# Optimization experiments

Hardware: AMD Instinct MI355X
Metric: run time of the kernel (lower is better)

## Reference

```python
import jax, jax.numpy as jnp
import numpy as np

# BiAttn: additive (concat-based) cross attention.
# Original torch: e = Linear([k_i ; q_j]) = k_i @ W[:H] + q_j @ W[H:] + b  (separable)
# a = softmax(e, axis=-1 over Y); out[b,x,h] = sum_y v[b,y,h] * a[b,x,y]

B, X, Y, H = 8, 2048, 2048, 1024


def setup_inputs() -> dict:
    key = jax.random.key(0)
    kq, kk, kv, kw = jax.random.split(key, 4)
    q = jax.random.normal(kq, (B, Y, H), dtype=jnp.float32)
    k = jax.random.normal(kk, (B, X, H), dtype=jnp.float32)
    v = jax.random.normal(kv, (B, Y, H), dtype=jnp.float32)
    W = jax.random.normal(kw, (2 * H,), dtype=jnp.float32) * (1.0 / np.sqrt(2 * H))
    b = jnp.zeros((), dtype=jnp.float32)
    return {"q": q, "k": k, "v": v, "W": W, "b": b}


def reference(q, k, v, W, b):
    Hdim = k.shape[-1]
    Wk, Wq = W[:Hdim], W[Hdim:]
    # Separable additive score: e[b,x,y] = k[b,x]@Wk + q[b,y]@Wq + b
    sk = jnp.einsum('bxh,h->bx', k, Wk)          # [B, X]
    sq = jnp.einsum('byh,h->by', q, Wq)          # [B, Y]
    e = sk[:, :, None] + sq[:, None, :] + b      # [B, X, Y]
    a = jax.nn.softmax(e, axis=-1)               # softmax over Y
    out = jnp.einsum('byh,bxy->bxh', v, a)       # [B, X, H]
    return out
```

## Files before the change

### kernel.cpp

```cpp
#include <hip/hip_runtime.h>

#define Bn 8
#define Xn 2048
#define Yn 2048
#define Hn 1024
#define YC 8
#define NCH (Yn / YC)

__global__ __launch_bounds__(256, 8)
void k_fused(const float* __restrict__ q, const float* __restrict__ W,
             const float* __restrict__ v,
             float* __restrict__ o_part, float* __restrict__ s_part) {
    const int b = blockIdx.y;
    const int c = blockIdx.x;
    const int y0 = c * YC;
    const int t = threadIdx.x;
    const int wave = t >> 6, lane = t & 63;
    __shared__ float pe[YC];

    const float4* w4 = (const float4*)(W + Hn);
    const float4 ww0 = w4[lane];
    const float4 ww1 = w4[lane + 64];
    const float4 ww2 = w4[lane + 128];
    const float4 ww3 = w4[lane + 192];

    {
        const int ra = wave * 2;
        const float4* qa = (const float4*)(q + ((size_t)b * Yn + y0 + ra) * Hn);
        const float4* qb = qa + (Hn / 4);
        float acca = 0.f, accb = 0.f;
        #pragma unroll
        for (int i = 0; i < 4; ++i) {
            float4 a  = qa[lane + 64 * i];
            float4 bb = qb[lane + 64 * i];
            float4 w  = (i == 0) ? ww0 : (i == 1) ? ww1 : (i == 2) ? ww2 : ww3;
            acca += a.x * w.x + a.y * w.y + a.z * w.z + a.w * w.w;
            accb += bb.x * w.x + bb.y * w.y + bb.z * w.z + bb.w * w.w;
        }
        #pragma unroll
        for (int off = 32; off > 0; off >>= 1) {
            acca += __shfl_xor(acca, off, 64);
            accb += __shfl_xor(accb, off, 64);
        }
        if (lane == 0) {
            pe[ra]     = __expf(acca);
            pe[ra + 1] = __expf(accb);
        }
    }
    __syncthreads();

    const float4* v4 = (const float4*)(v + ((size_t)b * Yn + y0) * Hn);
    float4 acc = {0.f, 0.f, 0.f, 0.f};
    #pragma unroll
    for (int yy = 0; yy < YC; ++yy) {
        const float pw = pe[yy];
        const float4 vv = v4[(size_t)yy * (Hn / 4) + t];
        acc.x = fmaf(pw, vv.x, acc.x);
        acc.y = fmaf(pw, vv.y, acc.y);
        acc.z = fmaf(pw, vv.z, acc.z);
        acc.w = fmaf(pw, vv.w, acc.w);
    }
    ((float4*)o_part)[((size_t)c * Bn + b) * (Hn / 4) + t] = acc;

    if (t == 0) {
        float s = 0.f;
        #pragma unroll
        for (int i = 0; i < YC; ++i) s += pe[i];
        s_part[c * Bn + b] = s;
    }
}

__global__ void k_red(const float* __restrict__ o_part,
                      const float* __restrict__ s_part,
                      float* __restrict__ o_final) {
    const int idx = blockIdx.x * 256 + threadIdx.x;
    const int b = idx >> 10;
    const int h = idx & (Hn - 1);
    float acc = 0.f, s = 0.f;
    #pragma unroll 8
    for (int c = 0; c < NCH; ++c) {
        acc += o_part[(size_t)(c * Bn + b) * Hn + h];
        s   += s_part[c * Bn + b];
    }
    o_final[idx] = acc / s;
}

__global__ void k_bcast(const float* __restrict__ o, float4* __restrict__ out) {
    const size_t i = (size_t)blockIdx.x * blockDim.x + threadIdx.x;
    const int h4 = (int)(i & (Hn / 4 - 1));
    const size_t row = i >> 8;
    const int b = (int)(row >> 11);
    const float4* o4 = (const float4*)o;
    out[i] = o4[b * (Hn / 4) + h4];
}

extern "C" void kernel_launch(void* const* d_in, const int* in_sizes, int n_in,
                              void* d_out, int out_size, void* d_ws, size_t ws_size,
                              hipStream_t stream) {
    const float* q = (const float*)d_in[0];
    const float* v = (const float*)d_in[2];
    const float* W = (const float*)d_in[3];
    float* out = (float*)d_out;

    float* o_part = (float*)d_ws;
    float* s_part = o_part + (size_t)NCH * Bn * Hn;
    float* o_fin  = s_part + NCH * Bn;

    k_fused<<<dim3(NCH, Bn), 256, 0, stream>>>(q, W, v, o_part, s_part);
    k_red  <<<Bn * Hn / 256, 256, 0, stream>>>(o_part, s_part, o_fin);
    k_bcast<<<(Bn * (size_t)Xn * Hn / 4) / 256, 256, 0, stream>>>(o_fin, (float4*)out);
}
```

Baseline: 216.9 us.

## Split score computation from PV accumulation and enlarge Y chunk per block

```diff
diff --git a/kernel.cpp b/kernel.cpp
--- a/kernel.cpp
+++ b/kernel.cpp
@@ -4,19 +4,18 @@
 #define Xn 2048
 #define Yn 2048
 #define Hn 1024
-#define YC 8
+#define RPB 8
+#define YC 32
 #define NCH (Yn / YC)
 
-__global__ __launch_bounds__(256, 8)
-void k_fused(const float* __restrict__ q, const float* __restrict__ W,
-             const float* __restrict__ v,
-             float* __restrict__ o_part, float* __restrict__ s_part) {
-    const int b = blockIdx.y;
-    const int c = blockIdx.x;
-    const int y0 = c * YC;
+
+__global__ __launch_bounds__(256)
+void k_pe(const float* __restrict__ q, const float* __restrict__ W,
+          float* __restrict__ pe, float* __restrict__ sb) {
+    const int blk = blockIdx.x;
     const int t = threadIdx.x;
     const int wave = t >> 6, lane = t & 63;
-    __shared__ float pe[YC];
+    __shared__ float ps[RPB];
 
     const float4* w4 = (const float4*)(W + Hn);
     const float4 ww0 = w4[lane];
@@ -24,65 +23,87 @@
     const float4 ww2 = w4[lane + 128];
     const float4 ww3 = w4[lane + 192];
 
-    {
-        const int ra = wave * 2;
-        const float4* qa = (const float4*)(q + ((size_t)b * Yn + y0 + ra) * Hn);
-        const float4* qb = qa + (Hn / 4);
-        float acca = 0.f, accb = 0.f;
+    const int ra = blk * RPB + wave * 2;
+    const float4* qa = (const float4*)(q + (size_t)ra * Hn);
+    const float4* qb = qa + (Hn / 4);
+    float acca = 0.f, accb = 0.f;
+    #pragma unroll
+    for (int i = 0; i < 4; ++i) {
+        float4 a  = qa[lane + 64 * i];
+        float4 bb = qb[lane + 64 * i];
+        float4 w  = (i == 0) ? ww0 : (i == 1) ? ww1 : (i == 2) ? ww2 : ww3;
+        acca += a.x * w.x + a.y * w.y + a.z * w.z + a.w * w.w;
+        accb += bb.x * w.x + bb.y * w.y + bb.z * w.z + bb.w * w.w;
+    }
+    #pragma unroll
+    for (int off = 32; off > 0; off >>= 1) {
+        acca += __shfl_xor(acca, off, 64);
+        accb += __shfl_xor(accb, off, 64);
+    }
+    if (lane == 0) {
+        float ea = __expf(acca), eb = __expf(accb);
+        pe[ra] = ea; pe[ra + 1] = eb;
+        ps[wave * 2] = ea; ps[wave * 2 + 1] = eb;
+    }
+    __syncthreads();
+    if (t == 0) {
+        float s = 0.f;
         #pragma unroll
-        for (int i = 0; i < 4; ++i) {
-            float4 a  = qa[lane + 64 * i];
-            float4 bb = qb[lane + 64 * i];
-            float4 w  = (i == 0) ? ww0 : (i == 1) ? ww1 : (i == 2) ? ww2 : ww3;
-            acca += a.x * w.x + a.y * w.y + a.z * w.z + a.w * w.w;
-            accb += bb.x * w.x + bb.y * w.y + bb.z * w.z + bb.w * w.w;
-        }
-        #pragma unroll
-        for (int off = 32; off > 0; off >>= 1) {
-            acca += __shfl_xor(acca, off, 64);
-            accb += __shfl_xor(accb, off, 64);
-        }
-        if (lane == 0) {
-            pe[ra]     = __expf(acca);
-            pe[ra + 1] = __expf(accb);
-        }
+        for (int i = 0; i < RPB; ++i) s += ps[i];
+        sb[blk] = s;
     }
+}
+
+__global__ __launch_bounds__(256)
+void k_pv(const float* __restrict__ v, const float* __restrict__ pe,
+          float* __restrict__ o_part) {
+    const int b = blockIdx.y;
+    const int c = blockIdx.x;
+    const int y0 = c * YC;
+    const int t = threadIdx.x;
+    __shared__ float pw[YC];
+    if (t < YC) pw[t] = pe[b * Yn + y0 + t];
     __syncthreads();
 
     const float4* v4 = (const float4*)(v + ((size_t)b * Yn + y0) * Hn);
     float4 acc = {0.f, 0.f, 0.f, 0.f};
-    #pragma unroll
+    #pragma unroll 16
     for (int yy = 0; yy < YC; ++yy) {
-        const float pw = pe[yy];
+        const float p = pw[yy];
         const float4 vv = v4[(size_t)yy * (Hn / 4) + t];
-        acc.x = fmaf(pw, vv.x, acc.x);
-        acc.y = fmaf(pw, vv.y, acc.y);
-        acc.z = fmaf(pw, vv.z, acc.z);
-        acc.w = fmaf(pw, vv.w, acc.w);
+        acc.x = fmaf(p, vv.x, acc.x);
+        acc.y = fmaf(p, vv.y, acc.y);
+        acc.z = fmaf(p, vv.z, acc.z);
+        acc.w = fmaf(p, vv.w, acc.w);
     }
     ((float4*)o_part)[((size_t)c * Bn + b) * (Hn / 4) + t] = acc;
-
-    if (t == 0) {
-        float s = 0.f;
-        #pragma unroll
-        for (int i = 0; i < YC; ++i) s += pe[i];
-        s_part[c * Bn + b] = s;
-    }
 }
 
-__global__ void k_red(const float* __restrict__ o_part,
-                      const float* __restrict__ s_part,
-                      float* __restrict__ o_final) {
-    const int idx = blockIdx.x * 256 + threadIdx.x;
-    const int b = idx >> 10;
-    const int h = idx & (Hn - 1);
-    float acc = 0.f, s = 0.f;
+__global__ __launch_bounds__(256)
+void k_red(const float* __restrict__ o_part, const float* __restrict__ sb,
+           float* __restrict__ o_final) {
+    const int b = blockIdx.x;
+    const int t = threadIdx.x;
+    const int wave = t >> 6, lane = t & 63;
+    __shared__ float wred[4];
+
+    float s = sb[b * (Yn / RPB) + t];
+    #pragma unroll
+    for (int off = 32; off > 0; off >>= 1) s += __shfl_xor(s, off, 64);
+    if (lane == 0) wred[wave] = s;
+    __syncthreads();
+    const float den = wred[0] + wred[1] + wred[2] + wred[3];
+    const float inv = 1.f / den;
+
+    float4 acc = {0.f, 0.f, 0.f, 0.f};
+    const float4* op4 = (const float4*)o_part;
     #pragma unroll 8
     for (int c = 0; c < NCH; ++c) {
-        acc += o_part[(size_t)(c * Bn + b) * Hn + h];
-        s   += s_part[c * Bn + b];
+        const float4 p = op4[((size_t)c * Bn + b) * (Hn / 4) + t];
+        acc.x += p.x; acc.y += p.y; acc.z += p.z; acc.w += p.w;
     }
-    o_final[idx] = acc / s;
+    acc.x *= inv; acc.y *= inv; acc.z *= inv; acc.w *= inv;
+    ((float4*)o_final)[b * (Hn / 4) + t] = acc;
 }
 
 __global__ void k_bcast(const float* __restrict__ o, float4* __restrict__ out) {
@@ -102,11 +123,13 @@
     const float* W = (const float*)d_in[3];
     float* out = (float*)d_out;
 
-    float* o_part = (float*)d_ws;
-    float* s_part = o_part + (size_t)NCH * Bn * Hn;
-    float* o_fin  = s_part + NCH * Bn;
+    float* pe     = (float*)d_ws;
+    float* sb     = pe + (size_t)Bn * Yn;
+    float* o_part = sb + Bn * Yn / RPB;
+    float* o_fin  = o_part + (size_t)NCH * Bn * Hn;
 
-    k_fused<<<dim3(NCH, Bn), 256, 0, stream>>>(q, W, v, o_part, s_part);
-    k_red  <<<Bn * Hn / 256, 256, 0, stream>>>(o_part, s_part, o_fin);
+    k_pe   <<<Bn * Yn / RPB, 256, 0, stream>>>(q, W, pe, sb);
+    k_pv   <<<dim3(NCH, Bn), 256, 0, stream>>>(v, pe, o_part);
+    k_red  <<<Bn, 256, 0, stream>>>(o_part, sb, o_fin);
     k_bcast<<<(Bn * (size_t)Xn * Hn / 4) / 256, 256, 0, stream>>>(o_fin, (float4*)out);
 }
```

Result: faster. 209.1 us (-3.6%).

## Double Y chunk, prefetch v rows before scores, and vectorize per-batch reduction

Applied to the files above, without the earlier changes.

```diff
diff --git a/kernel.cpp b/kernel.cpp
--- a/kernel.cpp
+++ b/kernel.cpp
@@ -4,10 +4,10 @@
 #define Xn 2048
 #define Yn 2048
 #define Hn 1024
-#define YC 8
+#define YC 16
 #define NCH (Yn / YC)
 
-__global__ __launch_bounds__(256, 8)
+__global__ __launch_bounds__(256)
 void k_fused(const float* __restrict__ q, const float* __restrict__ W,
              const float* __restrict__ v,
              float* __restrict__ o_part, float* __restrict__ s_part) {
@@ -18,49 +18,54 @@
     const int wave = t >> 6, lane = t & 63;
     __shared__ float pe[YC];
 
+    const float4* v4 = (const float4*)(v + ((size_t)b * Yn + y0) * Hn);
+    float4 vv[YC];
+    #pragma unroll
+    for (int yy = 0; yy < YC; ++yy)
+        vv[yy] = v4[(size_t)yy * (Hn / 4) + t];
+
     const float4* w4 = (const float4*)(W + Hn);
     const float4 ww0 = w4[lane];
     const float4 ww1 = w4[lane + 64];
     const float4 ww2 = w4[lane + 128];
     const float4 ww3 = w4[lane + 192];
 
-    {
-        const int ra = wave * 2;
-        const float4* qa = (const float4*)(q + ((size_t)b * Yn + y0 + ra) * Hn);
-        const float4* qb = qa + (Hn / 4);
-        float acca = 0.f, accb = 0.f;
+    const int r0 = wave * 4;
+    float acc[4];
+    #pragma unroll
+    for (int j = 0; j < 4; ++j) {
+        const float4* qr = (const float4*)(q + ((size_t)b * Yn + y0 + r0 + j) * Hn);
+        const float4 a0 = qr[lane];
+        const float4 a1 = qr[lane + 64];
+        const float4 a2 = qr[lane + 128];
+        const float4 a3 = qr[lane + 192];
+        float s;
+        s  = a0.x * ww0.x + a0.y * ww0.y + a0.z * ww0.z + a0.w * ww0.w;
+        s += a1.x * ww1.x + a1.y * ww1.y + a1.z * ww1.z + a1.w * ww1.w;
+        s += a2.x * ww2.x + a2.y * ww2.y + a2.z * ww2.z + a2.w * ww2.w;
+        s += a3.x * ww3.x + a3.y * ww3.y + a3.z * ww3.z + a3.w * ww3.w;
+        acc[j] = s;
+    }
+    #pragma unroll
+    for (int off = 32; off > 0; off >>= 1) {
         #pragma unroll
-        for (int i = 0; i < 4; ++i) {
-            float4 a  = qa[lane + 64 * i];
-            float4 bb = qb[lane + 64 * i];
-            float4 w  = (i == 0) ? ww0 : (i == 1) ? ww1 : (i == 2) ? ww2 : ww3;
-            acca += a.x * w.x + a.y * w.y + a.z * w.z + a.w * w.w;
-            accb += bb.x * w.x + bb.y * w.y + bb.z * w.z + bb.w * w.w;
-        }
-        #pragma unroll
-        for (int off = 32; off > 0; off >>= 1) {
-            acca += __shfl_xor(acca, off, 64);
-            accb += __shfl_xor(accb, off, 64);
-        }
-        if (lane == 0) {
-            pe[ra]     = __expf(acca);
-            pe[ra + 1] = __expf(accb);
-        }
+        for (int j = 0; j < 4; ++j)
+            acc[j] += __shfl_xor(acc[j], off, 64);
     }
+    if (lane < 4) pe[r0 + lane] = __expf(acc[lane]);
     __syncthreads();
 
-    const float4* v4 = (const float4*)(v + ((size_t)b * Yn + y0) * Hn);
-    float4 acc = {0.f, 0.f, 0.f, 0.f};
+
+    float4 o = {0.f, 0.f, 0.f, 0.f};
     #pragma unroll
     for (int yy = 0; yy < YC; ++yy) {
-        const float pw = pe[yy];
-        const float4 vv = v4[(size_t)yy * (Hn / 4) + t];
-        acc.x = fmaf(pw, vv.x, acc.x);
-        acc.y = fmaf(pw, vv.y, acc.y);
-        acc.z = fmaf(pw, vv.z, acc.z);
-        acc.w = fmaf(pw, vv.w, acc.w);
+        const float p = pe[yy];
+        o.x = fmaf(p, vv[yy].x, o.x);
+        o.y = fmaf(p, vv[yy].y, o.y);
+        o.z = fmaf(p, vv[yy].z, o.z);
+        o.w = fmaf(p, vv[yy].w, o.w);
     }
-    ((float4*)o_part)[((size_t)c * Bn + b) * (Hn / 4) + t] = acc;
+    ((float4*)o_part)[((size_t)c * Bn + b) * (Hn / 4) + t] = o;
 
     if (t == 0) {
         float s = 0.f;
@@ -70,19 +75,30 @@
     }
 }
 
-__global__ void k_red(const float* __restrict__ o_part,
-                      const float* __restrict__ s_part,
-                      float* __restrict__ o_final) {
-    const int idx = blockIdx.x * 256 + threadIdx.x;
-    const int b = idx >> 10;
-    const int h = idx & (Hn - 1);
-    float acc = 0.f, s = 0.f;
+__global__ __launch_bounds__(256)
+void k_red(const float* __restrict__ o_part, const float* __restrict__ s_part,
+           float* __restrict__ o_final) {
+    const int b = blockIdx.x;
+    const int t = threadIdx.x;
+    const int wave = t >> 6, lane = t & 63;
+    __shared__ float wred[4];
+
+    float s = (t < NCH) ? s_part[t * Bn + b] : 0.f;
+    #pragma unroll
+    for (int off = 32; off > 0; off >>= 1) s += __shfl_xor(s, off, 64);
+    if (lane == 0) wred[wave] = s;
+    __syncthreads();
+    const float inv = 1.f / (wred[0] + wred[1] + wred[2] + wred[3]);
+
+    float4 acc = {0.f, 0.f, 0.f, 0.f};
+    const float4* op4 = (const float4*)o_part;
     #pragma unroll 8
     for (int c = 0; c < NCH; ++c) {
-        acc += o_part[(size_t)(c * Bn + b) * Hn + h];
-        s   += s_part[c * Bn + b];
+        const float4 p = op4[((size_t)c * Bn + b) * (Hn / 4) + t];
+        acc.x += p.x; acc.y += p.y; acc.z += p.z; acc.w += p.w;
     }
-    o_final[idx] = acc / s;
+    acc.x *= inv; acc.y *= inv; acc.z *= inv; acc.w *= inv;
+    ((float4*)o_final)[b * (Hn / 4) + t] = acc;
 }
 
 __global__ void k_bcast(const float* __restrict__ o, float4* __restrict__ out) {
@@ -107,6 +123,6 @@
     float* o_fin  = s_part + NCH * Bn;
 
     k_fused<<<dim3(NCH, Bn), 256, 0, stream>>>(q, W, v, o_part, s_part);
-    k_red  <<<Bn * Hn / 256, 256, 0, stream>>>(o_part, s_part, o_fin);
+    k_red  <<<Bn, 256, 0, stream>>>(o_part, s_part, o_fin);
     k_bcast<<<(Bn * (size_t)Xn * Hn / 4) / 256, 256, 0, stream>>>(o_fin, (float4*)out);
 }
```

Result: faster. 211.8 us (-2.4%).
